# Kernel tuning notes

Measured on AMD Instinct MI355X. Metric: run time of the kernel, lower is better.

Reference implementation:

```python
import jax, jax.numpy as jnp
import numpy as np

NEG_INF = -9e15  # same masking constant as the original
LEAKY_ALPHA = 0.2  # tf.nn.leaky_relu default


def setup_inputs() -> dict:
    key = jax.random.key(0)
    k1, k2, k3, k4 = jax.random.split(key, 4)
    N, D, F = 8192, 256, 64
    features = jax.random.normal(k1, (N, D), dtype=jnp.float32)
    adj = jax.random.randint(k2, (N, N), 0, 2, dtype=jnp.int32)
    W = jax.random.normal(k3, (D, F), dtype=jnp.float32) * (1.0 / np.sqrt(D))
    a = jax.random.normal(k4, (2 * F, 1), dtype=jnp.float32) * 0.1
    return {"features": features, "adj": adj, "W": W, "a": a}


def reference(features, adj, W, a):
    # h = X W : [N, F]
    h = features @ W
    F = h.shape[1]
    # a^T [h_i || h_j] = (h a1)_i + (h a2)_j  -- avoids the N*N*2F concat tensor
    a1, a2 = a[:F], a[F:]            # [F,1] each
    e = jax.nn.leaky_relu((h @ a1) + (h @ a2).T, LEAKY_ALPHA)  # [N, N]
    scores = jnp.where(adj > 0, e, jnp.float32(NEG_INF))
    attention = jax.nn.softmax(scores, axis=1)                  # masked softmax over neighbors j
    h_prime = attention @ h                                     # [N, F]
    return jax.nn.elu(h_prime)
```

## Files before the change

### kernel.cpp

```cpp
#include <hip/hip_runtime.h>
#include <hip/hip_bf16.h>
#include <math.h>

#define NN 8192
#define DD 256
#define FF 64
#define WPB 4
#define ROWS 16
#define CPW (NN / 32 / WPB)

typedef __attribute__((ext_vector_type(8))) short bf16x8;
typedef __attribute__((ext_vector_type(4))) float f32x4;

__device__ __forceinline__ ushort f2bf(float x) {
  union { __hip_bfloat16 b; ushort s; } u;
  u.b = __float2bfloat16(x);
  return u.s;
}

__global__ __launch_bounds__(256) void k_pre(const float* __restrict__ W,
                                             ushort* __restrict__ WT) {
  const int e4 = (blockIdx.x * 256 + threadIdx.x) * 4;
  const float4 wv = *(const float4*)(W + e4);
  const int k = e4 >> 6, d = e4 & 63;
  WT[(d + 0) * DD + k] = f2bf(wv.x);
  WT[(d + 1) * DD + k] = f2bf(wv.y);
  WT[(d + 2) * DD + k] = f2bf(wv.z);
  WT[(d + 3) * DD + k] = f2bf(wv.w);
}

__global__ __launch_bounds__(256) void k_mask(const int* __restrict__ adj,
                                              uint* __restrict__ mask) {
  const size_t nquad = (size_t)NN * NN / 4;
  const size_t stride = (size_t)gridDim.x * 256;
  const int lane = threadIdx.x & 63;
  for (size_t q = (size_t)blockIdx.x * 256 + threadIdx.x; q < nquad; q += stride) {
    const int4 v = ((const int4*)adj)[q];
    uint nib = (uint)(v.x & 1) | ((uint)(v.y & 1) << 1) |
               ((uint)(v.z & 1) << 2) | ((uint)(v.w & 1) << 3);
    uint b = nib | ((uint)__shfl_xor((int)nib, 1) << 4);
    b |= (uint)__shfl_xor((int)b, 2) << 8;
    b |= (uint)__shfl_xor((int)b, 4) << 16;
    if ((lane & 7) == 0) mask[q >> 3] = b;
  }
}

__global__ __launch_bounds__(256) void k_h(
    const float* __restrict__ feat, const ushort* __restrict__ WT,
    const float* __restrict__ a, ushort* __restrict__ hTf,
    float* __restrict__ E1, float* __restrict__ F1,
    float* __restrict__ E2, float* __restrict__ F2) {
  __shared__ float sp1[4][16], sp2[4][16];
  const int t = threadIdx.x, lane = t & 63, w = t >> 6;
  const int il = lane & 15, kg = lane >> 4;
  const int ibase = blockIdx.x * 16;
  const int d = w * 16 + il;
  const float* frow = feat + (size_t)(ibase + il) * DD + kg * 8;
  const ushort* wrow = WT + (size_t)d * DD + kg * 8;
  f32x4 acc = {0.f, 0.f, 0.f, 0.f};
#pragma unroll
  for (int k0 = 0; k0 < DD; k0 += 32) {
    const float4 fa = *(const float4*)(frow + k0);
    const float4 fb = *(const float4*)(frow + k0 + 4);
    bf16x8 av;
    av[0] = f2bf(fa.x); av[1] = f2bf(fa.y); av[2] = f2bf(fa.z); av[3] = f2bf(fa.w);
    av[4] = f2bf(fb.x); av[5] = f2bf(fb.y); av[6] = f2bf(fb.z); av[7] = f2bf(fb.w);
    const bf16x8 bv = *(const bf16x8*)(wrow + k0);
    acc = __builtin_amdgcn_mfma_f32_16x16x32_bf16(av, bv, acc, 0, 0, 0);
  }
  ushort4 hv;
  hv.x = f2bf(acc[0]);
  hv.y = f2bf(acc[1]);
  hv.z = f2bf(acc[2]);
  hv.w = f2bf(acc[3]);
  {
    const int i0q = ibase + kg * 4;
    const size_t hb = ((size_t)(w * 256 + (i0q >> 5)) * 64 +
                       ((i0q >> 3) & 3) * 16 + il) * 8 + (i0q & 7);
    *(ushort4*)(hTf + hb) = hv;
  }
  const float a1v = a[d], a2v = a[FF + d];
#pragma unroll
  for (int r = 0; r < 4; ++r) {
    float v1 = acc[r] * a1v;
    float v2 = acc[r] * a2v;
#pragma unroll
    for (int m = 1; m <= 8; m <<= 1) {
      v1 += __shfl_xor(v1, m);
      v2 += __shfl_xor(v2, m);
    }
    if (il == 0) {
      sp1[w][kg * 4 + r] = v1;
      sp2[w][kg * 4 + r] = v2;
    }
  }
  __syncthreads();
  if (t < 16) {
    const float s1 = sp1[0][t] + sp1[1][t] + sp1[2][t] + sp1[3][t];
    const float s2 = sp2[0][t] + sp2[1][t] + sp2[2][t] + sp2[3][t];
    E1[ibase + t] = __expf(s1);
    F1[ibase + t] = __expf(0.2f * s1);
    E2[ibase + t] = __expf(s2);
    F2[ibase + t] = __expf(0.2f * s2);
  }
}

__global__ __launch_bounds__(256) void k_attn(
    const uint* __restrict__ mask, const ushort* __restrict__ hTf,
    const float* __restrict__ E1g, const float* __restrict__ F1g,
    const float* __restrict__ E2g, const float* __restrict__ F2g,
    float* __restrict__ out) {
  __shared__ float tr[WPB][16][65];
  __shared__ float lw[WPB][16];
  const int t = threadIdx.x;
  const int lane = t & 63, w = t >> 6;
  const int il = lane & 15, kg = lane >> 4;
  const int rbase = blockIdx.x * ROWS;
  const int row = rbase + il;
  const float e1 = E1g[row], f1 = F1g[row];
  const uint* mp = mask + (size_t)row * (NN / 32) + w * CPW;
  const int jb0 = w * CPW * 32 + kg * 8;

  bf16x8 ones;
#pragma unroll
  for (int e = 0; e < 8; ++e) ones[e] = (short)0x3F80;

  f32x4 acc[4] = {{0,0,0,0},{0,0,0,0},{0,0,0,0},{0,0,0,0}};
  f32x4 accl = {0.f, 0.f, 0.f, 0.f};

#pragma unroll 4
  for (int c = 0; c < CPW; ++c) {
    const uint bits = mp[c] >> (kg * 8);
    const int jo = jb0 + c * 32;
    const float4 e2a = *(const float4*)(E2g + jo);
    const float4 e2b = *(const float4*)(E2g + jo + 4);
    const float4 f2a = *(const float4*)(F2g + jo);
    const float4 f2b = *(const float4*)(F2g + jo + 4);
    bf16x8 pb;
    pb[0] = (bits & 1u)   ? (short)f2bf(fmaxf(e1 * e2a.x, f1 * f2a.x)) : (short)0;
    pb[1] = (bits & 2u)   ? (short)f2bf(fmaxf(e1 * e2a.y, f1 * f2a.y)) : (short)0;
    pb[2] = (bits & 4u)   ? (short)f2bf(fmaxf(e1 * e2a.z, f1 * f2a.z)) : (short)0;
    pb[3] = (bits & 8u)   ? (short)f2bf(fmaxf(e1 * e2a.w, f1 * f2a.w)) : (short)0;
    pb[4] = (bits & 16u)  ? (short)f2bf(fmaxf(e1 * e2b.x, f1 * f2b.x)) : (short)0;
    pb[5] = (bits & 32u)  ? (short)f2bf(fmaxf(e1 * e2b.y, f1 * f2b.y)) : (short)0;
    pb[6] = (bits & 64u)  ? (short)f2bf(fmaxf(e1 * e2b.z, f1 * f2b.z)) : (short)0;
    pb[7] = (bits & 128u) ? (short)f2bf(fmaxf(e1 * e2b.w, f1 * f2b.w)) : (short)0;
    accl = __builtin_amdgcn_mfma_f32_16x16x32_bf16(ones, pb, accl, 0, 0, 0);
    const int j32 = w * CPW + c;
#pragma unroll
    for (int f = 0; f < 4; ++f) {
      const bf16x8 hv =
          *(const bf16x8*)(hTf + ((size_t)(f * 256 + j32) * 64 + lane) * 8);
      acc[f] = __builtin_amdgcn_mfma_f32_16x16x32_bf16(hv, pb, acc[f], 0, 0, 0);
    }
  }
#pragma unroll
  for (int f = 0; f < 4; ++f)
#pragma unroll
    for (int r = 0; r < 4; ++r) tr[w][il][f * 16 + kg * 4 + r] = acc[f][r];
  if (lane < 16) lw[w][il] = accl[0];
  __syncthreads();
#pragma unroll
  for (int k = 0; k < (ROWS * FF) / 256; ++k) {
    const int idx = t + k * 256;
    const int r = idx >> 6, d = idx & 63;
    float s = 0.f, L = 0.f;
#pragma unroll
    for (int ww = 0; ww < WPB; ++ww) {
      s += tr[ww][r][d];
      L += lw[ww][r];
    }
    const float x = s / fmaxf(L, 1e-30f);
    out[(size_t)(rbase + r) * FF + d] = x > 0.f ? x : expm1f(x);
  }
}

extern "C" void kernel_launch(void* const* d_in, const int* in_sizes, int n_in,
                              void* d_out, int out_size, void* d_ws, size_t ws_size,
                              hipStream_t stream) {
  const float* feat = (const float*)d_in[0];
  const int* adj = (const int*)d_in[1];
  const float* W = (const float*)d_in[2];
  const float* a = (const float*)d_in[3];
  float* out = (float*)d_out;

  ushort* hTf = (ushort*)d_ws;
  ushort* WT = hTf + (size_t)FF * NN;
  float* E1 = (float*)(WT + (size_t)FF * DD);
  float* F1 = E1 + NN;
  float* E2 = F1 + NN;
  float* F2 = E2 + NN;
  uint* mask = (uint*)(F2 + NN);

  hipLaunchKernelGGL(k_pre, dim3(DD * FF / 1024), dim3(256), 0, stream, W, WT);
  hipLaunchKernelGGL(k_h, dim3(NN / 16), dim3(256), 0, stream, feat, WT, a, hTf,
                     E1, F1, E2, F2);
  hipLaunchKernelGGL(k_mask, dim3(2048), dim3(256), 0, stream, adj, mask);
  hipLaunchKernelGGL(k_attn, dim3(NN / ROWS), dim3(256), 0, stream,
                     mask, hTf, E1, F1, E2, F2, out);
}
```

Baseline: 442.4 us.

## Fuse adjacency bitmask packing into attention kernel via LDS staging

Removes the separate k_mask pass and has each attention block read its 16 rows of the int32 adjacency matrix directly, packing them into a bitmask held in shared memory (padded pitch) before the main loop. The attention block grows to 8 waves of 512 threads, so the column range is split further across waves. This removes the global bitmask write and re-read and one kernel launch. In exchange, the adjacency load is serialized ahead of the compute in each block, and the larger block adds LDS and register pressure.

```diff
diff --git a/kernel.cpp b/kernel.cpp
--- a/kernel.cpp
+++ b/kernel.cpp
@@ -5,9 +5,10 @@
 #define NN 8192
 #define DD 256
 #define FF 64
-#define WPB 4
+#define WPB 8
 #define ROWS 16
-#define CPW (NN / 32 / WPB)
+#define CPW 32
+#define MPITCH 257
 
 typedef __attribute__((ext_vector_type(8))) short bf16x8;
 typedef __attribute__((ext_vector_type(4))) float f32x4;
@@ -27,22 +28,6 @@
   WT[(d + 1) * DD + k] = f2bf(wv.y);
   WT[(d + 2) * DD + k] = f2bf(wv.z);
   WT[(d + 3) * DD + k] = f2bf(wv.w);
-}
-
-__global__ __launch_bounds__(256) void k_mask(const int* __restrict__ adj,
-                                              uint* __restrict__ mask) {
-  const size_t nquad = (size_t)NN * NN / 4;
-  const size_t stride = (size_t)gridDim.x * 256;
-  const int lane = threadIdx.x & 63;
-  for (size_t q = (size_t)blockIdx.x * 256 + threadIdx.x; q < nquad; q += stride) {
-    const int4 v = ((const int4*)adj)[q];
-    uint nib = (uint)(v.x & 1) | ((uint)(v.y & 1) << 1) |
-               ((uint)(v.z & 1) << 2) | ((uint)(v.w & 1) << 3);
-    uint b = nib | ((uint)__shfl_xor((int)nib, 1) << 4);
-    b |= (uint)__shfl_xor((int)b, 2) << 8;
-    b |= (uint)__shfl_xor((int)b, 4) << 16;
-    if ((lane & 7) == 0) mask[q >> 3] = b;
-  }
 }
 
 __global__ __launch_bounds__(256) void k_h(
@@ -105,11 +90,12 @@
   }
 }
 
-__global__ __launch_bounds__(256) void k_attn(
-    const uint* __restrict__ mask, const ushort* __restrict__ hTf,
+__global__ __launch_bounds__(512, 4) void k_attn(
+    const int* __restrict__ adj, const ushort* __restrict__ hTf,
     const float* __restrict__ E1g, const float* __restrict__ F1g,
     const float* __restrict__ E2g, const float* __restrict__ F2g,
     float* __restrict__ out) {
+  __shared__ uint maskL[ROWS][MPITCH];
   __shared__ float tr[WPB][16][65];
   __shared__ float lw[WPB][16];
   const int t = threadIdx.x;
@@ -117,20 +103,34 @@
   const int il = lane & 15, kg = lane >> 4;
   const int rbase = blockIdx.x * ROWS;
   const int row = rbase + il;
+
+  {
+    const int4* ap = (const int4*)(adj + (size_t)rbase * NN);
+#pragma unroll 4
+    for (int it = 0; it < (ROWS * NN / 4) / 512; ++it) {
+      const int qq = t + it * 512;
+      const int4 v = ap[qq];
+      uint nib = (uint)(v.x & 1) | ((uint)(v.y & 1) << 1) |
+                 ((uint)(v.z & 1) << 2) | ((uint)(v.w & 1) << 3);
+      uint b = nib | ((uint)__shfl_xor((int)nib, 1) << 4);
+      b |= (uint)__shfl_xor((int)b, 2) << 8;
+      b |= (uint)__shfl_xor((int)b, 4) << 16;
+      if ((lane & 7) == 0) maskL[qq >> 11][(qq >> 3) & 255] = b;
+    }
+  }
   const float e1 = E1g[row], f1 = F1g[row];
-  const uint* mp = mask + (size_t)row * (NN / 32) + w * CPW;
-  const int jb0 = w * CPW * 32 + kg * 8;
+  __syncthreads();
 
   bf16x8 ones;
 #pragma unroll
   for (int e = 0; e < 8; ++e) ones[e] = (short)0x3F80;
-
   f32x4 acc[4] = {{0,0,0,0},{0,0,0,0},{0,0,0,0},{0,0,0,0}};
   f32x4 accl = {0.f, 0.f, 0.f, 0.f};
+  const int jb0 = w * 1024 + kg * 8;
 
-#pragma unroll 4
+#pragma unroll 2
   for (int c = 0; c < CPW; ++c) {
-    const uint bits = mp[c] >> (kg * 8);
+    const uint bits = maskL[il][w * 32 + c] >> (kg * 8);
     const int jo = jb0 + c * 32;
     const float4 e2a = *(const float4*)(E2g + jo);
     const float4 e2b = *(const float4*)(E2g + jo + 4);
@@ -146,7 +146,7 @@
     pb[6] = (bits & 64u)  ? (short)f2bf(fmaxf(e1 * e2b.z, f1 * f2b.z)) : (short)0;
     pb[7] = (bits & 128u) ? (short)f2bf(fmaxf(e1 * e2b.w, f1 * f2b.w)) : (short)0;
     accl = __builtin_amdgcn_mfma_f32_16x16x32_bf16(ones, pb, accl, 0, 0, 0);
-    const int j32 = w * CPW + c;
+    const int j32 = w * 32 + c;
 #pragma unroll
     for (int f = 0; f < 4; ++f) {
       const bf16x8 hv =
@@ -161,8 +161,8 @@
   if (lane < 16) lw[w][il] = accl[0];
   __syncthreads();
 #pragma unroll
-  for (int k = 0; k < (ROWS * FF) / 256; ++k) {
-    const int idx = t + k * 256;
+  for (int k = 0; k < (ROWS * FF) / 512; ++k) {
+    const int idx = t + k * 512;
     const int r = idx >> 6, d = idx & 63;
     float s = 0.f, L = 0.f;
 #pragma unroll
@@ -190,12 +190,10 @@
   float* F1 = E1 + NN;
   float* E2 = F1 + NN;
   float* F2 = E2 + NN;
-  uint* mask = (uint*)(F2 + NN);
 
   hipLaunchKernelGGL(k_pre, dim3(DD * FF / 1024), dim3(256), 0, stream, W, WT);
   hipLaunchKernelGGL(k_h, dim3(NN / 16), dim3(256), 0, stream, feat, WT, a, hTf,
                      E1, F1, E2, F2);
-  hipLaunchKernelGGL(k_mask, dim3(2048), dim3(256), 0, stream, adj, mask);
-  hipLaunchKernelGGL(k_attn, dim3(NN / ROWS), dim3(256), 0, stream,
-                     mask, hTf, E1, F1, E2, F2, out);
+  hipLaunchKernelGGL(k_attn, dim3(NN / ROWS), dim3(512), 0, stream,
+                     adj, hTf, E1, F1, E2, F2, out);
 }
```

New measurement: 425.3 us. 3.9% less time.
